# Kernel tuning notes

Measured on AMD Instinct MI355X. Metric: run time of the kernel, lower is better.

## Reference

```python
import jax, jax.numpy as jnp
import numpy as np

N, E, H_DIM, HEADS = 20000, 640000, 128, 8
HD = H_DIM // HEADS  # head_dim = 16


def setup_inputs() -> dict:
    key = jax.random.key(0)
    ks = jax.random.split(key, 12)
    def xavier(k, shape):
        fan_in, fan_out = shape[0], shape[1]
        lim = jnp.sqrt(6.0 / (fan_in + fan_out))
        return jax.random.uniform(k, shape, jnp.float32, -lim, lim)
    return {
        "x": jax.random.normal(ks[0], (N, H_DIM), jnp.float32),
        "edge_index": jax.random.randint(ks[1], (2, E), 0, N, jnp.int64 if jax.config.x64_enabled else jnp.int32),
        "edge_attr": jax.random.normal(ks[2], (E, H_DIM), jnp.float32),
        "WQ": xavier(ks[3], (H_DIM, H_DIM)),
        "WK": xavier(ks[4], (H_DIM, H_DIM)),
        "WV": xavier(ks[5], (H_DIM, H_DIM)),
        "WE": xavier(ks[6], (H_DIM, H_DIM)),
        "Wout": xavier(ks[7], (H_DIM, H_DIM)),
        "bout": jnp.zeros((H_DIM,), jnp.float32),
        "gn_w": jnp.ones((H_DIM,), jnp.float32),
        "gn_b": jnp.zeros((H_DIM,), jnp.float32),
        "gn_ms": jnp.ones((H_DIM,), jnp.float32),
    }


def reference(x, edge_index, edge_attr, WQ, WK, WV, WE, Wout, bout, gn_w, gn_b, gn_ms):
    n = x.shape[0]
    src, dst = edge_index[0], edge_index[1]  # PyG: row=source j, col=target i

    q = (x @ WQ).reshape(n, HEADS, HD)
    k = (x @ WK).reshape(n, HEADS, HD)
    v = (x @ WV).reshape(n, HEADS, HD)
    e = (edge_attr @ WE).reshape(-1, HEADS, HD)

    # per-edge attention score [E, HEADS]
    score = jnp.sum(q[dst] * (k[src] + e), axis=-1) / jnp.sqrt(jnp.asarray(HD, x.dtype))

    # scatter-softmax over edges grouped by destination node
    seg_max = jax.ops.segment_max(score, dst, num_segments=n)  # [N, HEADS]
    seg_max = jnp.where(jnp.isfinite(seg_max), seg_max, 0.0)
    ex = jnp.exp(score - seg_max[dst])
    denom = jax.ops.segment_sum(ex, dst, num_segments=n)
    alpha = ex / (denom[dst] + 1e-16)  # [E, HEADS]

    # weighted scatter-add aggregation
    msg = alpha[..., None] * (v[src] + e)  # [E, HEADS, HD]
    out = jax.ops.segment_sum(msg, dst, num_segments=n).reshape(n, H_DIM)

    out = out @ Wout + bout
    h = out + x  # residual (DropPath is identity in eval)

    # GraphNorm with batch=None -> single-graph normalization
    mean = jnp.mean(h, axis=0)
    o = h - mean * gn_ms
    var = jnp.mean(o * o, axis=0)
    o = gn_w * o / jnp.sqrt(var + 1e-5) + gn_b

    return jax.nn.gelu(o, approximate=False)
```

## Files before the change

### kernel.cpp

```cpp
#include <hip/hip_runtime.h>

using u16 = unsigned short;
using u32 = unsigned int;
typedef float f32x4 __attribute__((ext_vector_type(4)));
typedef short s16x8 __attribute__((ext_vector_type(8)));
typedef u32   u32x2 __attribute__((ext_vector_type(2)));

__device__ __forceinline__ u16 f2bf(float f) {
  u32 u = __float_as_uint(f);
  u += 0x7fffu + ((u >> 16) & 1u);
  return (u16)(u >> 16);
}
__device__ __forceinline__ float bf2f(u16 h) {
  return __uint_as_float(((u32)h) << 16);
}

__global__ void ROEN_Final_33526514713351_kernel() {}


__global__ void roen_zero(int* __restrict__ count, int N, float* __restrict__ dbg) {
  int i = blockIdx.x * 256 + threadIdx.x;
  if (i == 0) dbg[0] = 1000.0f;
  if (i < N) count[i] = 0;
}

__global__ void roen_hist(const int* __restrict__ ei, int E, int* __restrict__ count,
                          float* __restrict__ dbg) {
  int i = blockIdx.x * 256 + threadIdx.x;
  if (i == 0) dbg[1] = 1001.0f;
  if (i < E) atomicAdd(&count[ei[E + i]], 1);
}

__global__ __launch_bounds__(256) void roen_scan(const int* __restrict__ count, int N,
                                                 int* __restrict__ off, int* __restrict__ cursor,
                                                 float* __restrict__ dbg) {
  __shared__ int tsum[256];
  int tid = threadIdx.x;
  if (tid == 0) dbg[2] = 1002.0f;
  int chunk = (N + 255) / 256;
  int b = tid * chunk;
  int e = b + chunk; if (e > N) e = N; if (b > N) b = N;
  int s = 0;
  for (int i = b; i < e; ++i) s += count[i];
  tsum[tid] = s;
  __syncthreads();
  for (int d = 1; d < 256; d <<= 1) {
    int t = (tid >= d) ? tsum[tid - d] : 0;
    __syncthreads();
    tsum[tid] += t;
    __syncthreads();
  }
  int run = tsum[tid] - s;
  for (int i = b; i < e; ++i) {
    off[i] = run; cursor[i] = run;
    run += count[i];
  }
  if (tid == 255) off[N] = run;
}

__global__ void roen_scatter(const int* __restrict__ ei, int E, int* __restrict__ cursor,
                             int* __restrict__ inv, int* __restrict__ srcS,
                             float* __restrict__ dbg) {
  int i = blockIdx.x * 256 + threadIdx.x;
  if (i == 0) dbg[3] = 1003.0f;
  if (i < E) {
    int s = ei[i];
    int d = ei[E + i];
    int p = atomicAdd(&cursor[d], 1);
    inv[i] = p;
    srcS[p] = s;
  }
}

__global__ void roen_prep_w(const float* __restrict__ W0, const float* __restrict__ W1,
                            const float* __restrict__ W2, const float* __restrict__ W3,
                            const float* __restrict__ W4, u16* __restrict__ Wt,
                            float* __restrict__ dbg) {
  int w = blockIdx.x;
  if (w == 0 && threadIdx.x == 0) dbg[4] = 1004.0f;
  const float* W = (w == 0) ? W0 : (w == 1) ? W1 : (w == 2) ? W2 : (w == 3) ? W3 : W4;
  for (int idx = threadIdx.x; idx < 16384; idx += 256) {
    int n = idx >> 7, k = idx & 127;
    Wt[w * 16384 + idx] = f2bf(W[k * 128 + n]);
  }
}

__global__ __launch_bounds__(256) void roen_gemm_qkv(const float* __restrict__ x,
                                                     const u16* __restrict__ Wt,
                                                     u16* __restrict__ qb, u16* __restrict__ kb,
                                                     u16* __restrict__ vb, int M,
                                                     float* __restrict__ dbg) {
  __shared__ u16 As[64 * 128];
  const int tid = threadIdx.x;
  if (blockIdx.x == 0 && tid == 0) dbg[5] = 1005.0f;
  const long brow = (long)blockIdx.x * 64;

  {
    f32x4 tmp[8];
#pragma unroll
    for (int j = 0; j < 8; ++j) {
      int idx = j * 256 + tid;
      int row = idx >> 5;
      int c4 = (idx & 31) * 4;
      long grow = brow + row;
      f32x4 a = {0.f, 0.f, 0.f, 0.f};
      if (grow < M) a = *(const f32x4*)(x + grow * 128 + c4);
      tmp[j] = a;
    }
#pragma unroll
    for (int j = 0; j < 8; ++j) {
      int idx = j * 256 + tid;
      int row = idx >> 5;
      int c4 = (idx & 31) * 4;
      u32 lo = ((u32)f2bf(tmp[j][1]) << 16) | (u32)f2bf(tmp[j][0]);
      u32 hi = ((u32)f2bf(tmp[j][3]) << 16) | (u32)f2bf(tmp[j][2]);
      int byte = (row * 256 + c4 * 2) ^ ((row & 7) << 4);
      u32x2 val; val[0] = lo; val[1] = hi;
      *(u32x2*)((char*)As + byte) = val;
    }
  }
  __syncthreads();

  const int wave = tid >> 6, lane = tid & 63;
  const int wc = wave * 32;
  const int lr = lane & 15, lg = lane >> 4;

  s16x8 af[4][4];
#pragma unroll
  for (int ks = 0; ks < 4; ++ks) {
    int kb2 = (ks * 32 + lg * 8) * 2;
#pragma unroll
    for (int mt = 0; mt < 4; ++mt) {
      int row = mt * 16 + lr;
      int byte = (row * 256 + kb2) ^ ((row & 7) << 4);
      af[ks][mt] = *(const s16x8*)((const char*)As + byte);
    }
  }

  for (int w = 0; w < 3; ++w) {
    s16x8 bfr[4][2];
#pragma unroll
    for (int ks = 0; ks < 4; ++ks)
#pragma unroll
      for (int nt = 0; nt < 2; ++nt)
        bfr[ks][nt] = *(const s16x8*)(Wt + w * 16384 + (wc + nt * 16 + lr) * 128 + ks * 32 + lg * 8);

    f32x4 acc[4][2];
    for (int mt = 0; mt < 4; ++mt)
      for (int nt = 0; nt < 2; ++nt) acc[mt][nt] = {0.f, 0.f, 0.f, 0.f};

#pragma unroll
    for (int ks = 0; ks < 4; ++ks)
      for (int mt = 0; mt < 4; ++mt)
        for (int nt = 0; nt < 2; ++nt)
          acc[mt][nt] = __builtin_amdgcn_mfma_f32_16x16x32_bf16(af[ks][mt], bfr[ks][nt], acc[mt][nt], 0, 0, 0);

    u16* C = (w == 0) ? qb : (w == 1) ? kb : vb;
    for (int mt = 0; mt < 4; ++mt) {
      for (int nt = 0; nt < 2; ++nt) {
        int col = wc + nt * 16 + lr;
        for (int r = 0; r < 4; ++r) {
          long row = brow + mt * 16 + lg * 4 + r;
          if (row < M) C[row * 128 + col] = f2bf(acc[mt][nt][r]);
        }
      }
    }
  }
}

__global__ __launch_bounds__(256) void roen_gemm_e(const float* __restrict__ ea,
                                                   const u16* __restrict__ WtE,
                                                   const int* __restrict__ inv,
                                                   const int* __restrict__ ei,
                                                   const u16* __restrict__ qb,
                                                   const u16* __restrict__ kb,
                                                   u16* __restrict__ eS,
                                                   float* __restrict__ wS, int E,
                                                   float* __restrict__ dbg) {
  __shared__ u16 As[128 * 128];
  __shared__ int invv[128];
  __shared__ int srcv[128];
  __shared__ int dstv[128];
  const int tid = threadIdx.x;
  if (blockIdx.x == 0 && tid == 0) dbg[6] = 1006.0f;
  const long brow = (long)blockIdx.x * 128;

  if (tid < 128) {
    long pos = brow + tid;
    invv[tid] = (pos < E) ? inv[pos] : -1;
    srcv[tid] = (pos < E) ? ei[pos] : 0;
  } else {
    long pos = brow + tid - 128;
    dstv[tid - 128] = (pos < E) ? ei[E + pos] : 0;
  }

  {
    f32x4 tmp[16];
#pragma unroll
    for (int j = 0; j < 16; ++j) {
      int idx = j * 256 + tid;
      int row = idx >> 5;
      int c4 = (idx & 31) * 4;
      long grow = brow + row;
      f32x4 a = {0.f, 0.f, 0.f, 0.f};
      if (grow < E) a = *(const f32x4*)(ea + grow * 128 + c4);
      tmp[j] = a;
    }
#pragma unroll
    for (int j = 0; j < 16; ++j) {
      int idx = j * 256 + tid;
      int row = idx >> 5;
      int c4 = (idx & 31) * 4;
      u32 lo = ((u32)f2bf(tmp[j][1]) << 16) | (u32)f2bf(tmp[j][0]);
      u32 hi = ((u32)f2bf(tmp[j][3]) << 16) | (u32)f2bf(tmp[j][2]);
      int byte = (row * 256 + c4 * 2) ^ ((row & 7) << 4);
      u32x2 val; val[0] = lo; val[1] = hi;
      *(u32x2*)((char*)As + byte) = val;
    }
  }

  const int wave = tid >> 6, lane = tid & 63;
  const int wc = wave * 32;
  const int lr = lane & 15, lg = lane >> 4;

  s16x8 bfr[4][2];
#pragma unroll
  for (int ks = 0; ks < 4; ++ks)
#pragma unroll
    for (int nt = 0; nt < 2; ++nt)
      bfr[ks][nt] = *(const s16x8*)(WtE + (wc + nt * 16 + lr) * 128 + ks * 32 + lg * 8);

  __syncthreads();

  f32x4 acc[8][2];
  for (int mt = 0; mt < 8; ++mt)
    for (int nt = 0; nt < 2; ++nt) acc[mt][nt] = {0.f, 0.f, 0.f, 0.f};

  for (int ks = 0; ks < 4; ++ks) {
    int kb2 = (ks * 32 + lg * 8) * 2;
    s16x8 af[8];
    for (int mt = 0; mt < 8; ++mt) {
      int row = mt * 16 + lr;
      int byte = (row * 256 + kb2) ^ ((row & 7) << 4);
      af[mt] = *(const s16x8*)((const char*)As + byte);
    }
    for (int mt = 0; mt < 8; ++mt)
      for (int nt = 0; nt < 2; ++nt)
        acc[mt][nt] = __builtin_amdgcn_mfma_f32_16x16x32_bf16(af[mt], bfr[ks][nt], acc[mt][nt], 0, 0, 0);
  }

  __syncthreads();
  for (int mt = 0; mt < 8; ++mt) {
    for (int nt = 0; nt < 2; ++nt) {
      int col = wc + nt * 16 + lr;
      for (int r = 0; r < 4; ++r) {
        int row = mt * 16 + lg * 4 + r;
        As[row * 128 + col] = f2bf(acc[mt][nt][r]);
      }
    }
  }
  __syncthreads();

  const int d0 = lane * 2;
  const int hh = lane >> 3;
  for (int rr = 0; rr < 32; ++rr) {
    int row = wave * 32 + rr;
    int op = invv[row];
    if (op < 0) continue;
    u32 ev = *(const u32*)((const char*)As + row * 256 + lane * 4);
    int src = srcv[row], dst = dstv[row];
    u32 qv = *(const u32*)(qb + (long)dst * 128 + d0);
    u32 kv = *(const u32*)(kb + (long)src * 128 + d0);
    float e0 = bf2f((u16)(ev & 0xffffu)), e1 = bf2f((u16)(ev >> 16));
    float p = bf2f((u16)(qv & 0xffffu)) * (bf2f((u16)(kv & 0xffffu)) + e0) +
              bf2f((u16)(qv >> 16)) * (bf2f((u16)(kv >> 16)) + e1);
    p += __shfl_xor(p, 1);
    p += __shfl_xor(p, 2);
    p += __shfl_xor(p, 4);
    if ((lane & 7) == 0) wS[(long)op * 8 + hh] = __expf(fminf(p * 0.25f, 80.f));
    *(u32*)(eS + (long)op * 128 + d0) = ev;
  }
}

__global__ __launch_bounds__(256) void roen_node_agg(const int* __restrict__ off,
                                                     const int* __restrict__ srcS,
                                                     const u16* __restrict__ eS,
                                                     const u16* __restrict__ vb,
                                                     const float* __restrict__ wS,
                                                     float* __restrict__ outat, int N,
                                                     float* __restrict__ dbg) {
  int wave = threadIdx.x >> 6;
  int lane = threadIdx.x & 63;
  int node = blockIdx.x * 4 + wave;
  if (node == 0 && lane == 0) dbg[10] = 1010.0f;
  if (node >= N) return;
  int beg = off[node], end = off[node + 1];

  const int d0 = lane * 2;
  const int hh = lane >> 3;
  float acc0 = 0.f, acc1 = 0.f, dsum = 0.f;

  int pos = beg;
  for (; pos + 4 <= end; pos += 4) {
    int s0 = srcS[pos], s1 = srcS[pos + 1], s2 = srcS[pos + 2], s3 = srcS[pos + 3];
    float w0 = wS[(long)(pos + 0) * 8 + hh];
    float w1 = wS[(long)(pos + 1) * 8 + hh];
    float w2 = wS[(long)(pos + 2) * 8 + hh];
    float w3 = wS[(long)(pos + 3) * 8 + hh];
    u32 e0 = *(const u32*)(eS + (long)(pos + 0) * 128 + d0);
    u32 e1 = *(const u32*)(eS + (long)(pos + 1) * 128 + d0);
    u32 e2 = *(const u32*)(eS + (long)(pos + 2) * 128 + d0);
    u32 e3 = *(const u32*)(eS + (long)(pos + 3) * 128 + d0);
    u32 v0 = *(const u32*)(vb + (long)s0 * 128 + d0);
    u32 v1 = *(const u32*)(vb + (long)s1 * 128 + d0);
    u32 v2 = *(const u32*)(vb + (long)s2 * 128 + d0);
    u32 v3 = *(const u32*)(vb + (long)s3 * 128 + d0);
    acc0 += w0 * (bf2f((u16)(v0 & 0xffffu)) + bf2f((u16)(e0 & 0xffffu)));
    acc1 += w0 * (bf2f((u16)(v0 >> 16)) + bf2f((u16)(e0 >> 16)));
    acc0 += w1 * (bf2f((u16)(v1 & 0xffffu)) + bf2f((u16)(e1 & 0xffffu)));
    acc1 += w1 * (bf2f((u16)(v1 >> 16)) + bf2f((u16)(e1 >> 16)));
    acc0 += w2 * (bf2f((u16)(v2 & 0xffffu)) + bf2f((u16)(e2 & 0xffffu)));
    acc1 += w2 * (bf2f((u16)(v2 >> 16)) + bf2f((u16)(e2 >> 16)));
    acc0 += w3 * (bf2f((u16)(v3 & 0xffffu)) + bf2f((u16)(e3 & 0xffffu)));
    acc1 += w3 * (bf2f((u16)(v3 >> 16)) + bf2f((u16)(e3 >> 16)));
    dsum += w0; dsum += w1; dsum += w2; dsum += w3;
  }
  for (; pos < end; ++pos) {
    float w = wS[(long)pos * 8 + hh];
    u32 ev = *(const u32*)(eS + (long)pos * 128 + d0);
    int src = srcS[pos];
    u32 vv = *(const u32*)(vb + (long)src * 128 + d0);
    acc0 += w * (bf2f((u16)(vv & 0xffffu)) + bf2f((u16)(ev & 0xffffu)));
    acc1 += w * (bf2f((u16)(vv >> 16)) + bf2f((u16)(ev >> 16)));
    dsum += w;
  }
  float inv = 1.f / (dsum + 1e-16f);
  outat[(long)node * 128 + d0] = acc0 * inv;
  outat[(long)node * 128 + d0 + 1] = acc1 * inv;
}

__global__ __launch_bounds__(256) void roen_gemm_out(const float* __restrict__ A,
                                                     const u16* __restrict__ Wt,
                                                     const float* __restrict__ x,
                                                     const float* __restrict__ bo,
                                                     float* __restrict__ h,
                                                     float* __restrict__ psum,
                                                     float* __restrict__ psumsq, int M,
                                                     float* __restrict__ dbg) {
  __shared__ u16 As[64 * 128];
  const int tid = threadIdx.x;
  if (blockIdx.x == 0 && tid == 0) dbg[11] = 1011.0f;
  const long brow = (long)blockIdx.x * 64;

  {
    f32x4 tmp[8];
#pragma unroll
    for (int j = 0; j < 8; ++j) {
      int idx = j * 256 + tid;
      int row = idx >> 5;
      int c4 = (idx & 31) * 4;
      long grow = brow + row;
      f32x4 a = {0.f, 0.f, 0.f, 0.f};
      if (grow < M) a = *(const f32x4*)(A + grow * 128 + c4);
      tmp[j] = a;
    }
#pragma unroll
    for (int j = 0; j < 8; ++j) {
      int idx = j * 256 + tid;
      int row = idx >> 5;
      int c4 = (idx & 31) * 4;
      u32 lo = ((u32)f2bf(tmp[j][1]) << 16) | (u32)f2bf(tmp[j][0]);
      u32 hi = ((u32)f2bf(tmp[j][3]) << 16) | (u32)f2bf(tmp[j][2]);
      int byte = (row * 256 + c4 * 2) ^ ((row & 7) << 4);
      u32x2 val; val[0] = lo; val[1] = hi;
      *(u32x2*)((char*)As + byte) = val;
    }
  }

  const int wave = tid >> 6, lane = tid & 63;
  const int wc = wave * 32;
  const int lr = lane & 15, lg = lane >> 4;

  s16x8 bfr[4][2];
#pragma unroll
  for (int ks = 0; ks < 4; ++ks)
#pragma unroll
    for (int nt = 0; nt < 2; ++nt)
      bfr[ks][nt] = *(const s16x8*)(Wt + (wc + nt * 16 + lr) * 128 + ks * 32 + lg * 8);

  __syncthreads();

  f32x4 acc[4][2];
  for (int mt = 0; mt < 4; ++mt)
    for (int nt = 0; nt < 2; ++nt) acc[mt][nt] = {0.f, 0.f, 0.f, 0.f};

  for (int ks = 0; ks < 4; ++ks) {
    int kb2 = (ks * 32 + lg * 8) * 2;
    s16x8 af[4];
    for (int mt = 0; mt < 4; ++mt) {
      int row = mt * 16 + lr;
      int byte = (row * 256 + kb2) ^ ((row & 7) << 4);
      af[mt] = *(const s16x8*)((const char*)As + byte);
    }
    for (int mt = 0; mt < 4; ++mt)
      for (int nt = 0; nt < 2; ++nt)
        acc[mt][nt] = __builtin_amdgcn_mfma_f32_16x16x32_bf16(af[mt], bfr[ks][nt], acc[mt][nt], 0, 0, 0);
  }

  float b0 = bo[wc + lr];
  float b1 = bo[wc + 16 + lr];
  float cs[2] = {0.f, 0.f}, cs2[2] = {0.f, 0.f};
  for (int mt = 0; mt < 4; ++mt) {
    for (int nt = 0; nt < 2; ++nt) {
      int col = wc + nt * 16 + lr;
      float bb = (nt == 0) ? b0 : b1;
      for (int r = 0; r < 4; ++r) {
        long row = brow + mt * 16 + lg * 4 + r;
        if (row < M) {
          long idx = row * 128 + col;
          float val = acc[mt][nt][r] + bb + x[idx];
          h[idx] = val;
          cs[nt] += val;
          cs2[nt] += val * val;
        }
      }
    }
  }
#pragma unroll
  for (int nt = 0; nt < 2; ++nt) {
    cs[nt] += __shfl_xor(cs[nt], 16);
    cs[nt] += __shfl_xor(cs[nt], 32);
    cs2[nt] += __shfl_xor(cs2[nt], 16);
    cs2[nt] += __shfl_xor(cs2[nt], 32);
  }
  if (lg == 0) {
    int col0 = wc + lr;
    psum[(long)blockIdx.x * 128 + col0] = cs[0];
    psumsq[(long)blockIdx.x * 128 + col0] = cs2[0];
    psum[(long)blockIdx.x * 128 + col0 + 16] = cs[1];
    psumsq[(long)blockIdx.x * 128 + col0 + 16] = cs2[1];
  }
}

__global__ void roen_stats(const float* __restrict__ psum, const float* __restrict__ psumsq,
                           const float* __restrict__ gnw, const float* __restrict__ gnb,
                           const float* __restrict__ gnms, float* __restrict__ Ac,
                           float* __restrict__ Bc, int nb, int N, float* __restrict__ dbg) {
  int d = threadIdx.x;
  if (d == 0) dbg[13] = 1013.0f;
  float s = 0.f, s2 = 0.f;
  for (int i = 0; i < nb; ++i) {
    s += psum[(long)i * 128 + d];
    s2 += psumsq[(long)i * 128 + d];
  }
  float mean = s / (float)N;
  float mm = mean * gnms[d];
  float var = s2 / (float)N - 2.f * mm * mean + mm * mm;
  float scale = gnw[d] * rsqrtf(var + 1e-5f);
  Ac[d] = scale;
  Bc[d] = gnb[d] - mm * scale;
}

__global__ __launch_bounds__(256) void roen_final(const float* __restrict__ h,
                                                  const float* __restrict__ Ac,
                                                  const float* __restrict__ Bc,
                                                  float* __restrict__ out, long total) {
  long i = (long)blockIdx.x * 256 + threadIdx.x;
  if (i >= total) return;
  int d = (int)(i & 127);
  float v = h[i] * Ac[d] + Bc[d];
  out[i] = 0.5f * v * (1.f + erff(v * 0.70710678f));
}

extern "C" void kernel_launch(void* const* d_in, const int* in_sizes, int n_in,
                              void* d_out, int out_size, void* d_ws, size_t ws_size,
                              hipStream_t stream) {
  const float* x   = (const float*)d_in[0];
  const int*   ei  = (const int*)d_in[1];
  const float* ea  = (const float*)d_in[2];
  const float* WQ  = (const float*)d_in[3];
  const float* WK  = (const float*)d_in[4];
  const float* WV  = (const float*)d_in[5];
  const float* WE  = (const float*)d_in[6];
  const float* Wo  = (const float*)d_in[7];
  const float* bo  = (const float*)d_in[8];
  const float* gnw = (const float*)d_in[9];
  const float* gnb = (const float*)d_in[10];
  const float* gnms= (const float*)d_in[11];
  float* out = (float*)d_out;
  float* dbg = (float*)d_out;

  const int N = in_sizes[0] / 128;
  const int E = in_sizes[1] / 2;
  const int gN = (N + 63) / 64;

  char* base = (char*)d_ws;
  size_t cur = 0;
  auto alloc = [&](size_t bytes) -> char* {
    char* r = base + cur;
    cur = (cur + bytes + 255) & ~(size_t)255;
    return r;
  };
  u16*   wt     = (u16*)alloc(5 * 16384 * sizeof(u16));
  u16*   qb     = (u16*)alloc((size_t)N * 128 * sizeof(u16));
  u16*   kb     = (u16*)alloc((size_t)N * 128 * sizeof(u16));
  u16*   vb     = (u16*)alloc((size_t)N * 128 * sizeof(u16));
  float* wS     = (float*)alloc((size_t)E * 8 * sizeof(float));
  int*   count  = (int*)alloc((size_t)N * sizeof(int));
  int*   offar  = (int*)alloc((size_t)(N + 1) * sizeof(int));
  int*   cursor = (int*)alloc((size_t)N * sizeof(int));
  int*   invar  = (int*)alloc((size_t)E * sizeof(int));
  int*   srcS   = (int*)alloc((size_t)E * sizeof(int));
  float* outat  = (float*)alloc((size_t)N * 128 * sizeof(float));
  float* psum   = (float*)alloc((size_t)gN * 128 * sizeof(float));
  float* psumsq = (float*)alloc((size_t)gN * 128 * sizeof(float));
  float* Ac     = (float*)alloc(128 * sizeof(float));
  float* Bc     = (float*)alloc(128 * sizeof(float));
  u16*   eS     = (u16*)alloc((size_t)E * 128 * sizeof(u16));
  float* hbuf   = (float*)eS;

  roen_zero<<<(N + 255) / 256, 256, 0, stream>>>(count, N, dbg);
  roen_hist<<<(E + 255) / 256, 256, 0, stream>>>(ei, E, count, dbg);
  roen_scan<<<1, 256, 0, stream>>>(count, N, offar, cursor, dbg);
  roen_scatter<<<(E + 255) / 256, 256, 0, stream>>>(ei, E, cursor, invar, srcS, dbg);
  roen_prep_w<<<5, 256, 0, stream>>>(WQ, WK, WV, WE, Wo, wt, dbg);

  roen_gemm_qkv<<<gN, 256, 0, stream>>>(x, wt, qb, kb, vb, N, dbg);
  roen_gemm_e<<<(E + 127) / 128, 256, 0, stream>>>(ea, wt + 3 * 16384, invar, ei, qb, kb, eS, wS, E, dbg);

  roen_node_agg<<<(N + 3) / 4, 256, 0, stream>>>(offar, srcS, eS, vb, wS, outat, N, dbg);

  roen_gemm_out<<<gN, 256, 0, stream>>>(outat, wt + 4 * 16384, x, bo, hbuf, psum, psumsq, N, dbg);
  roen_stats<<<1, 128, 0, stream>>>(psum, psumsq, gnw, gnb, gnms, Ac, Bc, gN, N, dbg);
  roen_final<<<(int)(((long)N * 128 + 255) / 256), 256, 0, stream>>>(hbuf, Ac, Bc, out, (long)N * 128);
}
```

Before: 502.7 us.

## Split edge score into separate kernel and pack e/v in MFMA-native layout

The edge GEMM no longer computes attention scores. It writes its bf16 output straight from MFMA accumulators into a packed u32 layout, scattered to sorted edge positions, which drops the LDS round trip and two syncs. A new roen_score kernel runs one thread per edge-head and gathers q/k through a new dstS array to compute exp-scores. V uses the same packed layout, so node_agg reads one u32 per lane holding two heads. This adds a kernel launch and a second pass over eS, in exchange for a leaner GEMM epilogue and coalesced stores.

```diff
diff --git a/kernel.cpp b/kernel.cpp
--- a/kernel.cpp
+++ b/kernel.cpp
@@ -5,6 +5,7 @@
 typedef float f32x4 __attribute__((ext_vector_type(4)));
 typedef short s16x8 __attribute__((ext_vector_type(8)));
 typedef u32   u32x2 __attribute__((ext_vector_type(2)));
+typedef u32   u32x4 __attribute__((ext_vector_type(4)));
 
 __device__ __forceinline__ u16 f2bf(float f) {
   u32 u = __float_as_uint(f);
@@ -60,7 +61,7 @@
 
 __global__ void roen_scatter(const int* __restrict__ ei, int E, int* __restrict__ cursor,
                              int* __restrict__ inv, int* __restrict__ srcS,
-                             float* __restrict__ dbg) {
+                             int* __restrict__ dstS, float* __restrict__ dbg) {
   int i = blockIdx.x * 256 + threadIdx.x;
   if (i == 0) dbg[3] = 1003.0f;
   if (i < E) {
@@ -69,6 +70,7 @@
     int p = atomicAdd(&cursor[d], 1);
     inv[i] = p;
     srcS[p] = s;
+    dstS[p] = d;
   }
 }
 
@@ -88,7 +90,7 @@
 __global__ __launch_bounds__(256) void roen_gemm_qkv(const float* __restrict__ x,
                                                      const u16* __restrict__ Wt,
                                                      u16* __restrict__ qb, u16* __restrict__ kb,
-                                                     u16* __restrict__ vb, int M,
+                                                     u32* __restrict__ vb2, int M,
                                                      float* __restrict__ dbg) {
   __shared__ u16 As[64 * 128];
   const int tid = threadIdx.x;
@@ -155,13 +157,25 @@
         for (int nt = 0; nt < 2; ++nt)
           acc[mt][nt] = __builtin_amdgcn_mfma_f32_16x16x32_bf16(af[ks][mt], bfr[ks][nt], acc[mt][nt], 0, 0, 0);
 
-    u16* C = (w == 0) ? qb : (w == 1) ? kb : vb;
-    for (int mt = 0; mt < 4; ++mt) {
-      for (int nt = 0; nt < 2; ++nt) {
-        int col = wc + nt * 16 + lr;
+    if (w == 2) {
+      for (int mt = 0; mt < 4; ++mt) {
         for (int r = 0; r < 4; ++r) {
           long row = brow + mt * 16 + lg * 4 + r;
-          if (row < M) C[row * 128 + col] = f2bf(acc[mt][nt][r]);
+          if (row < M) {
+            u32 val = (u32)f2bf(acc[mt][0][r]) | ((u32)f2bf(acc[mt][1][r]) << 16);
+            vb2[row * 64 + wave * 16 + lr] = val;
+          }
+        }
+      }
+    } else {
+      u16* C = (w == 0) ? qb : kb;
+      for (int mt = 0; mt < 4; ++mt) {
+        for (int nt = 0; nt < 2; ++nt) {
+          int col = wc + nt * 16 + lr;
+          for (int r = 0; r < 4; ++r) {
+            long row = brow + mt * 16 + lg * 4 + r;
+            if (row < M) C[row * 128 + col] = f2bf(acc[mt][nt][r]);
+          }
         }
       }
     }
@@ -171,16 +185,10 @@
 __global__ __launch_bounds__(256) void roen_gemm_e(const float* __restrict__ ea,
                                                    const u16* __restrict__ WtE,
                                                    const int* __restrict__ inv,
-                                                   const int* __restrict__ ei,
-                                                   const u16* __restrict__ qb,
-                                                   const u16* __restrict__ kb,
-                                                   u16* __restrict__ eS,
-                                                   float* __restrict__ wS, int E,
+                                                   u32* __restrict__ eS2, int E,
                                                    float* __restrict__ dbg) {
   __shared__ u16 As[128 * 128];
   __shared__ int invv[128];
-  __shared__ int srcv[128];
-  __shared__ int dstv[128];
   const int tid = threadIdx.x;
   if (blockIdx.x == 0 && tid == 0) dbg[6] = 1006.0f;
   const long brow = (long)blockIdx.x * 128;
@@ -188,10 +196,6 @@
   if (tid < 128) {
     long pos = brow + tid;
     invv[tid] = (pos < E) ? inv[pos] : -1;
-    srcv[tid] = (pos < E) ? ei[pos] : 0;
-  } else {
-    long pos = brow + tid - 128;
-    dstv[tid - 128] = (pos < E) ? ei[E + pos] : 0;
   }
 
   {
@@ -249,43 +253,55 @@
         acc[mt][nt] = __builtin_amdgcn_mfma_f32_16x16x32_bf16(af[mt], bfr[ks][nt], acc[mt][nt], 0, 0, 0);
   }
 
-  __syncthreads();
   for (int mt = 0; mt < 8; ++mt) {
-    for (int nt = 0; nt < 2; ++nt) {
-      int col = wc + nt * 16 + lr;
-      for (int r = 0; r < 4; ++r) {
-        int row = mt * 16 + lg * 4 + r;
-        As[row * 128 + col] = f2bf(acc[mt][nt][r]);
+    for (int r = 0; r < 4; ++r) {
+      int row = mt * 16 + lg * 4 + r;
+      int op = invv[row];
+      if (op >= 0) {
+        u32 val = (u32)f2bf(acc[mt][0][r]) | ((u32)f2bf(acc[mt][1][r]) << 16);
+        eS2[(long)op * 64 + wave * 16 + lr] = val;
       }
     }
   }
-  __syncthreads();
-
-  const int d0 = lane * 2;
-  const int hh = lane >> 3;
-  for (int rr = 0; rr < 32; ++rr) {
-    int row = wave * 32 + rr;
-    int op = invv[row];
-    if (op < 0) continue;
-    u32 ev = *(const u32*)((const char*)As + row * 256 + lane * 4);
-    int src = srcv[row], dst = dstv[row];
-    u32 qv = *(const u32*)(qb + (long)dst * 128 + d0);
-    u32 kv = *(const u32*)(kb + (long)src * 128 + d0);
-    float e0 = bf2f((u16)(ev & 0xffffu)), e1 = bf2f((u16)(ev >> 16));
-    float p = bf2f((u16)(qv & 0xffffu)) * (bf2f((u16)(kv & 0xffffu)) + e0) +
-              bf2f((u16)(qv >> 16)) * (bf2f((u16)(kv >> 16)) + e1);
-    p += __shfl_xor(p, 1);
-    p += __shfl_xor(p, 2);
-    p += __shfl_xor(p, 4);
-    if ((lane & 7) == 0) wS[(long)op * 8 + hh] = __expf(fminf(p * 0.25f, 80.f));
-    *(u32*)(eS + (long)op * 128 + d0) = ev;
-  }
+}
+
+__global__ __launch_bounds__(256) void roen_score(const int* __restrict__ srcS,
+                                                  const int* __restrict__ dstS,
+                                                  const u16* __restrict__ qb,
+                                                  const u16* __restrict__ kb,
+                                                  const u32* __restrict__ eS2,
+                                                  float* __restrict__ wS, int E,
+                                                  float* __restrict__ dbg) {
+  long gid = (long)blockIdx.x * 256 + threadIdx.x;
+  if (gid == 0) dbg[9] = 1009.0f;
+  long pos = gid >> 3;
+  int h = (int)(gid & 7);
+  if (pos >= E) return;
+  int dst = dstS[pos], src = srcS[pos];
+  const s16x8* qp = (const s16x8*)(qb + (long)dst * 128 + h * 16);
+  const s16x8* kp = (const s16x8*)(kb + (long)src * 128 + h * 16);
+  const u32x4* ep = (const u32x4*)(eS2 + (long)pos * 64 + (h >> 1) * 16);
+  const int sh = (h & 1) * 16;
+  float acc = 0.f;
+#pragma unroll
+  for (int c = 0; c < 2; ++c) {
+    s16x8 qv = qp[c], kv = kp[c];
+    u32x4 ea_ = ep[c * 2], eb_ = ep[c * 2 + 1];
+#pragma unroll
+    for (int j = 0; j < 4; ++j) {
+      float e0 = bf2f((u16)(ea_[j] >> sh));
+      float e1 = bf2f((u16)(eb_[j] >> sh));
+      acc += bf2f((u16)qv[j]) * (bf2f((u16)kv[j]) + e0);
+      acc += bf2f((u16)qv[j + 4]) * (bf2f((u16)kv[j + 4]) + e1);
+    }
+  }
+  wS[pos * 8 + h] = __expf(fminf(acc * 0.25f, 80.f));
 }
 
 __global__ __launch_bounds__(256) void roen_node_agg(const int* __restrict__ off,
                                                      const int* __restrict__ srcS,
-                                                     const u16* __restrict__ eS,
-                                                     const u16* __restrict__ vb,
+                                                     const u32* __restrict__ eS2,
+                                                     const u32* __restrict__ vb2,
                                                      const float* __restrict__ wS,
                                                      float* __restrict__ outat, int N,
                                                      float* __restrict__ dbg) {
@@ -296,47 +312,49 @@
   if (node >= N) return;
   int beg = off[node], end = off[node + 1];
 
-  const int d0 = lane * 2;
-  const int hh = lane >> 3;
-  float acc0 = 0.f, acc1 = 0.f, dsum = 0.f;
+  const int dA = 32 * (lane >> 4) + (lane & 15);
+  const int dB = dA + 16;
+  const int hA = dA >> 4;
+  const int hB = hA + 1;
+  float accA = 0.f, accB = 0.f, dsA = 0.f, dsB = 0.f;
 
   int pos = beg;
   for (; pos + 4 <= end; pos += 4) {
     int s0 = srcS[pos], s1 = srcS[pos + 1], s2 = srcS[pos + 2], s3 = srcS[pos + 3];
-    float w0 = wS[(long)(pos + 0) * 8 + hh];
-    float w1 = wS[(long)(pos + 1) * 8 + hh];
-    float w2 = wS[(long)(pos + 2) * 8 + hh];
-    float w3 = wS[(long)(pos + 3) * 8 + hh];
-    u32 e0 = *(const u32*)(eS + (long)(pos + 0) * 128 + d0);
-    u32 e1 = *(const u32*)(eS + (long)(pos + 1) * 128 + d0);
-    u32 e2 = *(const u32*)(eS + (long)(pos + 2) * 128 + d0);
-    u32 e3 = *(const u32*)(eS + (long)(pos + 3) * 128 + d0);
-    u32 v0 = *(const u32*)(vb + (long)s0 * 128 + d0);
-    u32 v1 = *(const u32*)(vb + (long)s1 * 128 + d0);
-    u32 v2 = *(const u32*)(vb + (long)s2 * 128 + d0);
-    u32 v3 = *(const u32*)(vb + (long)s3 * 128 + d0);
-    acc0 += w0 * (bf2f((u16)(v0 & 0xffffu)) + bf2f((u16)(e0 & 0xffffu)));
-    acc1 += w0 * (bf2f((u16)(v0 >> 16)) + bf2f((u16)(e0 >> 16)));
-    acc0 += w1 * (bf2f((u16)(v1 & 0xffffu)) + bf2f((u16)(e1 & 0xffffu)));
-    acc1 += w1 * (bf2f((u16)(v1 >> 16)) + bf2f((u16)(e1 >> 16)));
-    acc0 += w2 * (bf2f((u16)(v2 & 0xffffu)) + bf2f((u16)(e2 & 0xffffu)));
-    acc1 += w2 * (bf2f((u16)(v2 >> 16)) + bf2f((u16)(e2 >> 16)));
-    acc0 += w3 * (bf2f((u16)(v3 & 0xffffu)) + bf2f((u16)(e3 & 0xffffu)));
-    acc1 += w3 * (bf2f((u16)(v3 >> 16)) + bf2f((u16)(e3 >> 16)));
-    dsum += w0; dsum += w1; dsum += w2; dsum += w3;
+    float wa0 = wS[(long)(pos + 0) * 8 + hA], wb0 = wS[(long)(pos + 0) * 8 + hB];
+    float wa1 = wS[(long)(pos + 1) * 8 + hA], wb1 = wS[(long)(pos + 1) * 8 + hB];
+    float wa2 = wS[(long)(pos + 2) * 8 + hA], wb2 = wS[(long)(pos + 2) * 8 + hB];
+    float wa3 = wS[(long)(pos + 3) * 8 + hA], wb3 = wS[(long)(pos + 3) * 8 + hB];
+    u32 e0 = eS2[(long)(pos + 0) * 64 + lane];
+    u32 e1 = eS2[(long)(pos + 1) * 64 + lane];
+    u32 e2 = eS2[(long)(pos + 2) * 64 + lane];
+    u32 e3 = eS2[(long)(pos + 3) * 64 + lane];
+    u32 v0 = vb2[(long)s0 * 64 + lane];
+    u32 v1 = vb2[(long)s1 * 64 + lane];
+    u32 v2 = vb2[(long)s2 * 64 + lane];
+    u32 v3 = vb2[(long)s3 * 64 + lane];
+    accA += wa0 * (bf2f((u16)v0) + bf2f((u16)e0));
+    accB += wb0 * (bf2f((u16)(v0 >> 16)) + bf2f((u16)(e0 >> 16)));
+    accA += wa1 * (bf2f((u16)v1) + bf2f((u16)e1));
+    accB += wb1 * (bf2f((u16)(v1 >> 16)) + bf2f((u16)(e1 >> 16)));
+    accA += wa2 * (bf2f((u16)v2) + bf2f((u16)e2));
+    accB += wb2 * (bf2f((u16)(v2 >> 16)) + bf2f((u16)(e2 >> 16)));
+    accA += wa3 * (bf2f((u16)v3) + bf2f((u16)e3));
+    accB += wb3 * (bf2f((u16)(v3 >> 16)) + bf2f((u16)(e3 >> 16)));
+    dsA += wa0 + wa1 + wa2 + wa3;
+    dsB += wb0 + wb1 + wb2 + wb3;
   }
   for (; pos < end; ++pos) {
-    float w = wS[(long)pos * 8 + hh];
-    u32 ev = *(const u32*)(eS + (long)pos * 128 + d0);
+    float wa = wS[(long)pos * 8 + hA], wb = wS[(long)pos * 8 + hB];
+    u32 ev = eS2[(long)pos * 64 + lane];
     int src = srcS[pos];
-    u32 vv = *(const u32*)(vb + (long)src * 128 + d0);
-    acc0 += w * (bf2f((u16)(vv & 0xffffu)) + bf2f((u16)(ev & 0xffffu)));
-    acc1 += w * (bf2f((u16)(vv >> 16)) + bf2f((u16)(ev >> 16)));
-    dsum += w;
-  }
-  float inv = 1.f / (dsum + 1e-16f);
-  outat[(long)node * 128 + d0] = acc0 * inv;
-  outat[(long)node * 128 + d0 + 1] = acc1 * inv;
+    u32 vv = vb2[(long)src * 64 + lane];
+    accA += wa * (bf2f((u16)vv) + bf2f((u16)ev));
+    accB += wb * (bf2f((u16)(vv >> 16)) + bf2f((u16)(ev >> 16)));
+    dsA += wa; dsB += wb;
+  }
+  outat[(long)node * 128 + dA] = accA / (dsA + 1e-16f);
+  outat[(long)node * 128 + dB] = accB / (dsB + 1e-16f);
 }
 
 __global__ __launch_bounds__(256) void roen_gemm_out(const float* __restrict__ A,
@@ -504,31 +522,33 @@
   u16*   wt     = (u16*)alloc(5 * 16384 * sizeof(u16));
   u16*   qb     = (u16*)alloc((size_t)N * 128 * sizeof(u16));
   u16*   kb     = (u16*)alloc((size_t)N * 128 * sizeof(u16));
-  u16*   vb     = (u16*)alloc((size_t)N * 128 * sizeof(u16));
+  u32*   vb2    = (u32*)alloc((size_t)N * 64 * sizeof(u32));
   float* wS     = (float*)alloc((size_t)E * 8 * sizeof(float));
   int*   count  = (int*)alloc((size_t)N * sizeof(int));
   int*   offar  = (int*)alloc((size_t)(N + 1) * sizeof(int));
   int*   cursor = (int*)alloc((size_t)N * sizeof(int));
   int*   invar  = (int*)alloc((size_t)E * sizeof(int));
   int*   srcS   = (int*)alloc((size_t)E * sizeof(int));
+  int*   dstS   = (int*)alloc((size_t)E * sizeof(int));
   float* outat  = (float*)alloc((size_t)N * 128 * sizeof(float));
   float* psum   = (float*)alloc((size_t)gN * 128 * sizeof(float));
   float* psumsq = (float*)alloc((size_t)gN * 128 * sizeof(float));
   float* Ac     = (float*)alloc(128 * sizeof(float));
   float* Bc     = (float*)alloc(128 * sizeof(float));
-  u16*   eS     = (u16*)alloc((size_t)E * 128 * sizeof(u16));
-  float* hbuf   = (float*)eS;
+  u32*   eS2    = (u32*)alloc((size_t)E * 64 * sizeof(u32));
+  float* hbuf   = (float*)eS2;
 
   roen_zero<<<(N + 255) / 256, 256, 0, stream>>>(count, N, dbg);
   roen_hist<<<(E + 255) / 256, 256, 0, stream>>>(ei, E, count, dbg);
   roen_scan<<<1, 256, 0, stream>>>(count, N, offar, cursor, dbg);
-  roen_scatter<<<(E + 255) / 256, 256, 0, stream>>>(ei, E, cursor, invar, srcS, dbg);
+  roen_scatter<<<(E + 255) / 256, 256, 0, stream>>>(ei, E, cursor, invar, srcS, dstS, dbg);
   roen_prep_w<<<5, 256, 0, stream>>>(WQ, WK, WV, WE, Wo, wt, dbg);
 
-  roen_gemm_qkv<<<gN, 256, 0, stream>>>(x, wt, qb, kb, vb, N, dbg);
-  roen_gemm_e<<<(E + 127) / 128, 256, 0, stream>>>(ea, wt + 3 * 16384, invar, ei, qb, kb, eS, wS, E, dbg);
-
-  roen_node_agg<<<(N + 3) / 4, 256, 0, stream>>>(offar, srcS, eS, vb, wS, outat, N, dbg);
+  roen_gemm_qkv<<<gN, 256, 0, stream>>>(x, wt, qb, kb, vb2, N, dbg);
+  roen_gemm_e<<<(E + 127) / 128, 256, 0, stream>>>(ea, wt + 3 * 16384, invar, eS2, E, dbg);
+
+  roen_score<<<(int)(((long)E * 8 + 255) / 256), 256, 0, stream>>>(srcS, dstS, qb, kb, eS2, wS, E, dbg);
+  roen_node_agg<<<(N + 3) / 4, 256, 0, stream>>>(offar, srcS, eS2, vb2, wS, outat, N, dbg);
 
   roen_gemm_out<<<gN, 256, 0, stream>>>(outat, wt + 4 * 16384, x, bo, hbuf, psum, psumsq, N, dbg);
   roen_stats<<<1, 128, 0, stream>>>(psum, psumsq, gnw, gnb, gnms, Ac, Bc, gN, N, dbg);
```

After: 457.6 us. -9.0%, faster.
